# Kernel optimization log

Hardware: AMD Instinct MI355X
Metric: run time of the kernel (lower is better)

## Reference

```python
import jax, jax.numpy as jnp
import numpy as np
from jax import lax

MAX_SIGMA = 20.0
TRUNCATE = 4.0  # scipy.ndimage.gaussian_filter default
R = int(TRUNCATE * MAX_SIGMA + 0.5)  # fixed max radius = 80 -> 161 taps


def setup_inputs() -> dict:
    key = jax.random.key(0)
    k1, k2 = jax.random.split(key)
    x = jax.random.normal(k1, (512, 256, 256), dtype=jnp.float32)
    blur_sigmas = jnp.geomspace(0.5, MAX_SIGMA, 32).astype(jnp.float32)
    fwd_steps = jax.random.randint(k2, (512,), 0, 32)
    return {"x": x, "blur_sigmas": blur_sigmas, "fwd_steps": fwd_steps}


def _per_sample_kernels(sigmas):
    # scipy gaussian_filter: radius_i = int(truncate*sigma + 0.5), kernel
    # phi(o) = exp(-o^2 / (2 sigma^2)) normalized over |o| <= radius_i.
    off = jnp.arange(-R, R + 1, dtype=jnp.float32)          # [2R+1]
    w = jnp.exp(-0.5 * (off[None, :] / sigmas[:, None]) ** 2)  # [B, 2R+1]
    rad = jnp.floor(TRUNCATE * sigmas + 0.5)[:, None]        # per-sample radius
    w = w * (jnp.abs(off)[None, :] <= rad)
    return w / jnp.sum(w, axis=-1, keepdims=True)


def _blur(x, kernels):
    # x: [B, H, W]; kernels: [B, 2R+1]. Separable depthwise conv, batch as
    # channels with feature_group_count=B; symmetric pad == scipy 'reflect'.
    B = x.shape[0]
    dn = ("NCHW", "OIHW", "NCHW")
    xp = jnp.pad(x, ((0, 0), (R, R), (R, R)), mode="symmetric")[None]  # [1,B,H+2R,W+2R]
    kh = kernels[:, None, :, None]  # [B,1,2R+1,1]
    kw = kernels[:, None, None, :]  # [B,1,1,2R+1]
    y = lax.conv_general_dilated(xp, kh, (1, 1), "VALID",
                                 dimension_numbers=dn, feature_group_count=B)
    y = lax.conv_general_dilated(y, kw, (1, 1), "VALID",
                                 dimension_numbers=dn, feature_group_count=B)
    return y[0]  # [B, H, W]


def reference(x, blur_sigmas, fwd_steps):
    sigmas = blur_sigmas[fwd_steps]           # [B] per-sample sigma
    kernels = _per_sample_kernels(sigmas)     # [B, 2R+1]
    return _blur(x, kernels)
```

## Files before the change

### kernel.cpp

```cpp
#include <hip/hip_runtime.h>

#define WDIM  256
#define NSAMP 512
#define NSIG  32
#define NBLK  2048
#define QOFF  16
#define WOFF  65536

typedef float    f32x4 __attribute__((ext_vector_type(4)));
typedef _Float16 f16x4 __attribute__((ext_vector_type(4)));
typedef _Float16 f16x8 __attribute__((ext_vector_type(8)));
typedef __fp16   fp16x2 __attribute__((ext_vector_type(2)));

#define LDS_BARRIER() do {                                         \
    asm volatile("s_waitcnt lgkmcnt(0)" ::: "memory");             \
    __builtin_amdgcn_s_barrier();                                  \
} while (0)

__device__ __forceinline__ int reflect(int q) {
    q = (q < 0) ? (-q - 1) : q;
    return (q >= WDIM) ? (2 * WDIM - 1 - q) : q;
}

__global__ __launch_bounds__(256) void build_all(const float* __restrict__ sigmas,
                                                 const int* __restrict__ steps,
                                                 _Float16* __restrict__ Wg,
                                                 int* __restrict__ q) {
    int t = threadIdx.x;
    if (blockIdx.x < 256) {
        __shared__ float wl[161];
        __shared__ float red;
        int s = blockIdx.x >> 3, og = blockIdx.x & 7;
        float sigma = sigmas[s];
        float radf = floorf(4.0f * sigma + 0.5f);
        if (t < 161) {
            float off = (float)(t - 80);
            float w = 0.0f;
            if (fabsf(off) <= radf) { float z = off / sigma; w = expf(-0.5f * z * z); }
            wl[t] = w;
        }
        __syncthreads();
        if (t < 64) {
            float v = wl[t] + wl[t + 64] + (t < 33 ? wl[t + 128] : 0.0f);
            #pragma unroll
            for (int o = 32; o > 0; o >>= 1) v += __shfl_down(v, o);
            if (t == 0) red = 1.0f / v;
        }
        __syncthreads();
        float rs = red;
        int i = t;
        _Float16* wrow = Wg + ((size_t)s << 16) + (i << 8);
        for (int rq = og * 4; rq < og * 4 + 4; ++rq) {
            f16x8 v;
            #pragma unroll
            for (int j = 0; j < 8; ++j) {
                int r = rq * 8 + j;
                int d1 = r - i, d2 = -r - 1 - i, d3 = 511 - r - i;
                float w = 0.0f;
                if (d1 >= -80 && d1 <= 80) w += wl[d1 + 80];
                if (d2 >= -80)             w += wl[d2 + 80];
                if (d3 <= 80)              w += wl[d3 + 80];
                v[j] = (_Float16)(w * rs);
            }
            *(f16x8*)(wrow + rq * 8) = v;
        }
    } else {
        __shared__ int hist[32];
        __shared__ int base[32];
        if (t < 32) hist[t] = 0;
        __syncthreads();
        int nb2[2], rd2[2], st2[2];
        #pragma unroll
        for (int k = 0; k < 2; ++k) {
            int samp = t + 256 * k;
            int st = steps[samp];
            float sigma = sigmas[st];
            int rad = (int)floorf(4.0f * sigma + 0.5f);
            st2[k] = st; rd2[k] = rad;
            nb2[k] = (2 * rad + 15) >> 3;
            atomicAdd(&hist[nb2[k]], 1);
        }
        __syncthreads();
        if (t == 0) {
            int acc = 0;
            for (int bin = 31; bin >= 0; --bin) { base[bin] = acc; acc += hist[bin]; }
        }
        __syncthreads();
        #pragma unroll
        for (int k = 0; k < 2; ++k) {
            int samp = t + 256 * k;
            int r = atomicAdd(&base[nb2[k]], 1);
            int x = r & 7;
            int p = r >> 3;
            #pragma unroll
            for (int jb = 0; jb < 4; ++jb)
                q[QOFF + (((p << 2) + jb) << 3) + x] =
                    samp | (jb << 9) | (st2[k] << 11) | (rd2[k] << 16);
        }
    }
}

template <bool QUEUED>
__global__ __launch_bounds__(256, 3) void blur_mfma(const float* __restrict__ in,
                                                    float* __restrict__ out,
                                                    const float* __restrict__ sigmas,
                                                    const int* __restrict__ steps,
                                                    const int* __restrict__ q,
                                                    const _Float16* __restrict__ Wg) {
    __shared__ alignas(16) _Float16 XL[256 * 32];
    __shared__ alignas(16) _Float16 WH[64 * 32];
    __shared__ alignas(16) _Float16 YT[64 * 256];

    int b, j0, s, rad;
    if constexpr (QUEUED) {
        int d = q[QOFF + blockIdx.x];
        b   = d & 511;
        j0  = ((d >> 9) & 3) << 6;
        s   = (d >> 11) & 31;
        rad = (d >> 16) & 127;
    } else {
        int bid = blockIdx.x;
        int e = (bid & 7) * (NBLK / 8) + (bid >> 3);
        b = e >> 2; j0 = (e & 3) << 6;
        s = steps[b];
        rad = (int)floorf(4.0f * sigmas[s] + 0.5f);
    }
    const _Float16* Wm = Wg + ((size_t)s << 16);
    const float*    Xb = in + ((size_t)b << 16);

    int tt = threadIdx.x;
    int ln = tt & 63, wv = tt >> 6;
    int lm = ln & 15, lq = ln >> 4;

    int sr = tt >> 3;
    int sc = (tt & 7) * 4;
    int sj = tt >> 2;
    int sw8 = (tt & 3) * 8;

    int kh0 = max(0, j0 - rad) >> 5;
    int kh1 = min(WDIM - 1, j0 + 63 + rad) >> 5;

    f32x4 xs[8];
    f16x8 wst;
    auto ldstage = [&](int kt) {
        const float* xp = Xb + (size_t)sr * WDIM + (kt << 5) + sc;
        #pragma unroll
        for (int k = 0; k < 8; ++k)
            xs[k] = *(const f32x4*)(xp + (size_t)(k * 32) * WDIM);
        wst = *(const f16x8*)(Wm + (size_t)(j0 + sj) * WDIM + (kt << 5) + sw8);
    };
    auto wrstage = [&]() {
        #pragma unroll
        for (int k = 0; k < 8; ++k) {
            int rr = sr + 32 * k;
            union { f16x4 v; fp16x2 h[2]; } u;
            u.h[0] = __builtin_amdgcn_cvt_pkrtz(xs[k][0], xs[k][1]);
            u.h[1] = __builtin_amdgcn_cvt_pkrtz(xs[k][2], xs[k][3]);
            *(f16x4*)&XL[rr * 32 + ((((sc >> 3) ^ (rr & 3)) << 3) + (sc & 7))] = u.v;
        }
        *(f16x8*)&WH[sj * 32 + (((tt & 3) ^ (sj & 3)) << 3)] = wst;
    };

    f32x4 acc[4][4];
    #pragma unroll
    for (int mt = 0; mt < 4; ++mt)
        #pragma unroll
        for (int nt = 0; nt < 4; ++nt) acc[mt][nt] = (f32x4)0.0f;

    ldstage(kh0);
    for (int kt = kh0; kt <= kh1; ++kt) {
        wrstage();
        LDS_BARRIER();
        if (kt < kh1) ldstage(kt + 1);
        f16x8 bf[4];
        #pragma unroll
        for (int nt = 0; nt < 4; ++nt) {
            int j = nt * 16 + lm;
            bf[nt] = *(const f16x8*)&WH[j * 32 + ((lq ^ (j & 3)) << 3)];
        }
        #pragma unroll
        for (int mt = 0; mt < 4; ++mt) {
            int r = wv * 64 + mt * 16 + lm;
            f16x8 af = *(const f16x8*)&XL[r * 32 + ((lq ^ (r & 3)) << 3)];
            #pragma unroll
            for (int nt = 0; nt < 4; ++nt)
                acc[mt][nt] = __builtin_amdgcn_mfma_f32_16x16x32_f16(af, bf[nt], acc[mt][nt], 0, 0, 0);
        }
        LDS_BARRIER();
    }

    #pragma unroll
    for (int mt = 0; mt < 4; ++mt)
        #pragma unroll
        for (int nt = 0; nt < 4; ++nt) {
            int r4 = wv * 64 + mt * 16 + lq * 4;
            int j  = nt * 16 + lm;
            union { f16x4 v; fp16x2 h[2]; } u;
            u.h[0] = __builtin_amdgcn_cvt_pkrtz(acc[mt][nt][0], acc[mt][nt][1]);
            u.h[1] = __builtin_amdgcn_cvt_pkrtz(acc[mt][nt][2], acc[mt][nt][3]);
            *(f16x4*)&YT[j * 256 + ((((r4 >> 3) ^ (j & 7)) << 3) + (r4 & 7))] = u.v;
        }
    LDS_BARRIER();

    f32x4 hac[4][4];
    #pragma unroll
    for (int mt = 0; mt < 4; ++mt)
        #pragma unroll
        for (int nt = 0; nt < 4; ++nt) hac[mt][nt] = (f32x4)0.0f;

    int ka[4], kb[4];
    #pragma unroll
    for (int mt = 0; mt < 4; ++mt) {
        int i0m = wv * 64 + mt * 16;
        ka[mt] = max(0, i0m - rad) >> 5;
        kb[mt] = min(WDIM - 1, i0m + 15 + rad) >> 5;
    }

    for (int kt = ka[0]; kt <= kb[3]; ++kt) {
        f16x8 bf[4];
        #pragma unroll
        for (int nt = 0; nt < 4; ++nt) {
            int j = nt * 16 + lm;
            bf[nt] = *(const f16x8*)&YT[j * 256 + ((((kt << 2) + lq) ^ (j & 7)) << 3)];
        }
        #pragma unroll
        for (int mt = 0; mt < 4; ++mt) {
            if (kt >= ka[mt] && kt <= kb[mt]) {
                f16x8 af = *(const f16x8*)(Wm + (size_t)(wv * 64 + mt * 16 + lm) * WDIM + (kt << 5) + lq * 8);
                #pragma unroll
                for (int nt = 0; nt < 4; ++nt)
                    hac[mt][nt] = __builtin_amdgcn_mfma_f32_16x16x32_f16(af, bf[nt], hac[mt][nt], 0, 0, 0);
            }
        }
    }

    float* ob = out + ((size_t)b << 16);
    #pragma unroll
    for (int mt = 0; mt < 4; ++mt)
        #pragma unroll
        for (int nt = 0; nt < 4; ++nt)
            #pragma unroll
            for (int g = 0; g < 4; ++g)
                ob[(size_t)(wv * 64 + mt * 16 + lq * 4 + g) * WDIM + j0 + nt * 16 + lm] = hac[mt][nt][g];
}

__device__ __forceinline__ int make_weights161(int b, const float* __restrict__ sigmas,
                                               const int* __restrict__ steps,
                                               float* wl, float* red) {
    int t = threadIdx.x;
    float sigma = sigmas[steps[b]];
    float radf = floorf(4.0f * sigma + 0.5f);
    if (t < 192) {
        float w = 0.0f;
        if (t < 161) {
            float off = (float)(t - 80);
            if (fabsf(off) <= radf) { float z = off / sigma; w = expf(-0.5f * z * z); }
        }
        wl[t] = w;
    }
    __syncthreads();
    if (t < 64) {
        float v = wl[t] + wl[t + 64] + wl[t + 128];
        #pragma unroll
        for (int o = 32; o > 0; o >>= 1) v += __shfl_down(v, o);
        if (t == 0) red[0] = 1.0f / v;
    }
    __syncthreads();
    float rs = red[0];
    if (t < 161) wl[t] *= rs;
    __syncthreads();
    return (int)radf;
}

__global__ __launch_bounds__(256) void vblur_nt(const float* __restrict__ in,
                                                float* __restrict__ out,
                                                const float* __restrict__ sigmas,
                                                const int* __restrict__ steps) {
    __shared__ float wl[192];
    __shared__ float red[1];
    int bid = blockIdx.x;
    int b = bid >> 4, i0 = (bid & 15) * 16;
    int rad = make_weights161(b, sigmas, steps, wl, red);
    int j = threadIdx.x;
    const float* inb = in + (size_t)b * WDIM * WDIM;
    float acc[16];
    #pragma unroll
    for (int ii = 0; ii < 16; ++ii) acc[ii] = 0.0f;
    for (int u = -rad; u <= rad; ++u) {
        float w = wl[80 + u];
        #pragma unroll
        for (int ii = 0; ii < 16; ++ii)
            acc[ii] = fmaf(w, inb[reflect(i0 + ii + u) * WDIM + j], acc[ii]);
    }
    #pragma unroll
    for (int ii = 0; ii < 16; ++ii)
        out[((size_t)b * WDIM + (i0 + ii)) * WDIM + j] = acc[ii];
}

__global__ __launch_bounds__(256) void hblur_inplace(float* __restrict__ buf,
                                                     const float* __restrict__ sigmas,
                                                     const int* __restrict__ steps) {
    __shared__ float wl[192];
    __shared__ float red[1];
    __shared__ float rp[WDIM + 160];
    int bid = blockIdx.x;
    int b = bid >> 8, i = bid & 255;
    float* row = buf + ((size_t)b * WDIM + i) * WDIM;
    int t = threadIdx.x;
    for (int s = t; s < WDIM + 160; s += 256) rp[s] = row[reflect(s - 80)];
    int rad = make_weights161(b, sigmas, steps, wl, red);
    float acc = 0.0f;
    for (int u = -rad; u <= rad; ++u) acc = fmaf(wl[80 + u], rp[80 + t + u], acc);
    row[t] = acc;
}

extern "C" void kernel_launch(void* const* d_in, const int* in_sizes, int n_in,
                              void* d_out, int out_size, void* d_ws, size_t ws_size,
                              hipStream_t stream) {
    const float* x     = (const float*)d_in[0];
    const float* sig   = (const float*)d_in[1];
    const int*   steps = (const int*)d_in[2];
    float* out = (float*)d_out;

    const size_t need = (size_t)WOFF + (size_t)NSIG * WDIM * WDIM * 2;
    if (ws_size >= need) {
        int* q = (int*)d_ws;
        _Float16* Wg = (_Float16*)((char*)d_ws + WOFF);
        build_all<<<257, 256, 0, stream>>>(sig, steps, Wg, q);
        blur_mfma<true><<<NBLK, 256, 0, stream>>>(x, out, sig, steps, q, Wg);
    } else {
        vblur_nt<<<NSAMP * 16, 256, 0, stream>>>(x, out, sig, steps);
        hblur_inplace<<<NSAMP * WDIM, 256, 0, stream>>>(out, sig, steps);
    }
}
```

Baseline: 73.62 us.

## Split fused blur into separate horizontal and vertical MFMA kernels via fp16 workspace

The single fused kernel, which kept the horizontal-pass result in LDS and then ran the vertical pass on it, is split into two kernels. The first writes an fp16 intermediate to a global workspace, and the second reads it back to run the vertical pass over its own row tile. Removing the large YT LDS buffer lowers shared-memory use, which allows higher occupancy (launch bounds raised to 4 blocks per CU). In exchange it adds a global round trip of 64 MB (written and read) and a second kernel launch, and it needs a larger workspace; if the workspace is too small, the slow scalar fallback path runs instead.

```diff
diff --git a/kernel.cpp b/kernel.cpp
--- a/kernel.cpp
+++ b/kernel.cpp
@@ -6,6 +6,7 @@
 #define NBLK  2048
 #define QOFF  16
 #define WOFF  65536
+#define TOFF  (WOFF + NSIG * WDIM * WDIM * 2)
 
 typedef float    f32x4 __attribute__((ext_vector_type(4)));
 typedef _Float16 f16x4 __attribute__((ext_vector_type(4)));
@@ -101,23 +102,19 @@
 }
 
 template <bool QUEUED>
-__global__ __launch_bounds__(256, 3) void blur_mfma(const float* __restrict__ in,
-                                                    float* __restrict__ out,
-                                                    const float* __restrict__ sigmas,
-                                                    const int* __restrict__ steps,
-                                                    const int* __restrict__ q,
-                                                    const _Float16* __restrict__ Wg) {
+__global__ __launch_bounds__(256, 4) void blur_h(const float* __restrict__ in,
+                                                 _Float16* __restrict__ tmp,
+                                                 const float* __restrict__ sigmas,
+                                                 const int* __restrict__ steps,
+                                                 const int* __restrict__ q,
+                                                 const _Float16* __restrict__ Wg) {
     __shared__ alignas(16) _Float16 XL[256 * 32];
     __shared__ alignas(16) _Float16 WH[64 * 32];
-    __shared__ alignas(16) _Float16 YT[64 * 256];
 
     int b, j0, s, rad;
     if constexpr (QUEUED) {
         int d = q[QOFF + blockIdx.x];
-        b   = d & 511;
-        j0  = ((d >> 9) & 3) << 6;
-        s   = (d >> 11) & 31;
-        rad = (d >> 16) & 127;
+        b = d & 511; j0 = ((d >> 9) & 3) << 6; s = (d >> 11) & 31; rad = (d >> 16) & 127;
     } else {
         int bid = blockIdx.x;
         int e = (bid & 7) * (NBLK / 8) + (bid >> 3);
@@ -131,7 +128,6 @@
     int tt = threadIdx.x;
     int ln = tt & 63, wv = tt >> 6;
     int lm = ln & 15, lq = ln >> 4;
-
     int sr = tt >> 3;
     int sc = (tt & 7) * 4;
     int sj = tt >> 2;
@@ -189,18 +185,44 @@
         LDS_BARRIER();
     }
 
+    _Float16* tb = tmp + ((size_t)b << 16);
     #pragma unroll
     for (int mt = 0; mt < 4; ++mt)
         #pragma unroll
         for (int nt = 0; nt < 4; ++nt) {
             int r4 = wv * 64 + mt * 16 + lq * 4;
-            int j  = nt * 16 + lm;
+            int j  = j0 + nt * 16 + lm;
             union { f16x4 v; fp16x2 h[2]; } u;
             u.h[0] = __builtin_amdgcn_cvt_pkrtz(acc[mt][nt][0], acc[mt][nt][1]);
             u.h[1] = __builtin_amdgcn_cvt_pkrtz(acc[mt][nt][2], acc[mt][nt][3]);
-            *(f16x4*)&YT[j * 256 + ((((r4 >> 3) ^ (j & 7)) << 3) + (r4 & 7))] = u.v;
-        }
-    LDS_BARRIER();
+            *(f16x4*)&tb[(j << 8) + r4] = u.v;
+        }
+}
+
+template <bool QUEUED>
+__global__ __launch_bounds__(256, 4) void blur_v(const _Float16* __restrict__ tmp,
+                                                 float* __restrict__ out,
+                                                 const float* __restrict__ sigmas,
+                                                 const int* __restrict__ steps,
+                                                 const int* __restrict__ q,
+                                                 const _Float16* __restrict__ Wg) {
+    int b, i0, s, rad;
+    if constexpr (QUEUED) {
+        int d = q[QOFF + blockIdx.x];
+        b = d & 511; i0 = ((d >> 9) & 3) << 6; s = (d >> 11) & 31; rad = (d >> 16) & 127;
+    } else {
+        int bid = blockIdx.x;
+        int e = (bid & 7) * (NBLK / 8) + (bid >> 3);
+        b = e >> 2; i0 = (e & 3) << 6;
+        s = steps[b];
+        rad = (int)floorf(4.0f * sigmas[s] + 0.5f);
+    }
+    const _Float16* Wm = Wg + ((size_t)s << 16);
+    const _Float16* tb = tmp + ((size_t)b << 16);
+
+    int ln = threadIdx.x & 63, wv = threadIdx.x >> 6;
+    int lm = ln & 15, lq = ln >> 4;
+    int jlo = wv * 64;
 
     f32x4 hac[4][4];
     #pragma unroll
@@ -211,22 +233,22 @@
     int ka[4], kb[4];
     #pragma unroll
     for (int mt = 0; mt < 4; ++mt) {
-        int i0m = wv * 64 + mt * 16;
-        ka[mt] = max(0, i0m - rad) >> 5;
-        kb[mt] = min(WDIM - 1, i0m + 15 + rad) >> 5;
+        int im = i0 + mt * 16;
+        ka[mt] = max(0, im - rad) >> 5;
+        kb[mt] = min(WDIM - 1, im + 15 + rad) >> 5;
     }
 
     for (int kt = ka[0]; kt <= kb[3]; ++kt) {
         f16x8 bf[4];
         #pragma unroll
         for (int nt = 0; nt < 4; ++nt) {
-            int j = nt * 16 + lm;
-            bf[nt] = *(const f16x8*)&YT[j * 256 + ((((kt << 2) + lq) ^ (j & 7)) << 3)];
+            int j = jlo + nt * 16 + lm;
+            bf[nt] = *(const f16x8*)&tb[(j << 8) + (kt << 5) + lq * 8];
         }
         #pragma unroll
         for (int mt = 0; mt < 4; ++mt) {
             if (kt >= ka[mt] && kt <= kb[mt]) {
-                f16x8 af = *(const f16x8*)(Wm + (size_t)(wv * 64 + mt * 16 + lm) * WDIM + (kt << 5) + lq * 8);
+                f16x8 af = *(const f16x8*)(Wm + (size_t)(i0 + mt * 16 + lm) * WDIM + (kt << 5) + lq * 8);
                 #pragma unroll
                 for (int nt = 0; nt < 4; ++nt)
                     hac[mt][nt] = __builtin_amdgcn_mfma_f32_16x16x32_f16(af, bf[nt], hac[mt][nt], 0, 0, 0);
@@ -241,7 +263,7 @@
         for (int nt = 0; nt < 4; ++nt)
             #pragma unroll
             for (int g = 0; g < 4; ++g)
-                ob[(size_t)(wv * 64 + mt * 16 + lq * 4 + g) * WDIM + j0 + nt * 16 + lm] = hac[mt][nt][g];
+                ob[(size_t)(i0 + mt * 16 + lq * 4 + g) * WDIM + jlo + nt * 16 + lm] = hac[mt][nt][g];
 }
 
 __device__ __forceinline__ int make_weights161(int b, const float* __restrict__ sigmas,
@@ -322,12 +344,14 @@
     const int*   steps = (const int*)d_in[2];
     float* out = (float*)d_out;
 
-    const size_t need = (size_t)WOFF + (size_t)NSIG * WDIM * WDIM * 2;
+    const size_t need = (size_t)TOFF + (size_t)NSAMP * WDIM * WDIM * 2;
     if (ws_size >= need) {
         int* q = (int*)d_ws;
-        _Float16* Wg = (_Float16*)((char*)d_ws + WOFF);
+        _Float16* Wg  = (_Float16*)((char*)d_ws + WOFF);
+        _Float16* tmp = (_Float16*)((char*)d_ws + TOFF);
         build_all<<<257, 256, 0, stream>>>(sig, steps, Wg, q);
-        blur_mfma<true><<<NBLK, 256, 0, stream>>>(x, out, sig, steps, q, Wg);
+        blur_h<true><<<NBLK, 256, 0, stream>>>(x, tmp, sig, steps, q, Wg);
+        blur_v<true><<<NBLK, 256, 0, stream>>>(tmp, out, sig, steps, q, Wg);
     } else {
         vblur_nt<<<NSAMP * 16, 256, 0, stream>>>(x, out, sig, steps);
         hblur_inplace<<<NSAMP * WDIM, 256, 0, stream>>>(out, sig, steps);
```

Measured after the change: 124.5 us. 1.69x slower.

## Load MFMA operands directly from global memory, dropping LDS staging in first pass

Applied to the files above, without the earlier changes.

The first (vertical-as-GEMM) pass now loads the input rows and the per-sigma weight matrix straight from global memory into MFMA operand registers, instead of staging them through XL/WH shared buffers with double-buffered prefetch and barriers. This removes LDS writes, two barriers per k-tile and 5 KB+ of LDS, which may raise occupancy. In exchange, the software prefetch overlap is lost, each wave issues its own uncoalesced-ish 32-byte row reads, and the weight tile is read redundantly by all four waves, so it leans on the cache.

```diff
diff --git a/kernel.cpp b/kernel.cpp
--- a/kernel.cpp
+++ b/kernel.cpp
@@ -107,17 +107,12 @@
                                                     const int* __restrict__ steps,
                                                     const int* __restrict__ q,
                                                     const _Float16* __restrict__ Wg) {
-    __shared__ alignas(16) _Float16 XL[256 * 32];
-    __shared__ alignas(16) _Float16 WH[64 * 32];
     __shared__ alignas(16) _Float16 YT[64 * 256];
 
     int b, j0, s, rad;
     if constexpr (QUEUED) {
         int d = q[QOFF + blockIdx.x];
-        b   = d & 511;
-        j0  = ((d >> 9) & 3) << 6;
-        s   = (d >> 11) & 31;
-        rad = (d >> 16) & 127;
+        b = d & 511; j0 = ((d >> 9) & 3) << 6; s = (d >> 11) & 31; rad = (d >> 16) & 127;
     } else {
         int bid = blockIdx.x;
         int e = (bid & 7) * (NBLK / 8) + (bid >> 3);
@@ -128,65 +123,41 @@
     const _Float16* Wm = Wg + ((size_t)s << 16);
     const float*    Xb = in + ((size_t)b << 16);
 
-    int tt = threadIdx.x;
-    int ln = tt & 63, wv = tt >> 6;
+    int ln = threadIdx.x & 63, wv = threadIdx.x >> 6;
     int lm = ln & 15, lq = ln >> 4;
 
-    int sr = tt >> 3;
-    int sc = (tt & 7) * 4;
-    int sj = tt >> 2;
-    int sw8 = (tt & 3) * 8;
+    f32x4 acc[4][4];
+    #pragma unroll
+    for (int mt = 0; mt < 4; ++mt)
+        #pragma unroll
+        for (int nt = 0; nt < 4; ++nt) acc[mt][nt] = (f32x4)0.0f;
 
     int kh0 = max(0, j0 - rad) >> 5;
     int kh1 = min(WDIM - 1, j0 + 63 + rad) >> 5;
 
-    f32x4 xs[8];
-    f16x8 wst;
-    auto ldstage = [&](int kt) {
-        const float* xp = Xb + (size_t)sr * WDIM + (kt << 5) + sc;
-        #pragma unroll
-        for (int k = 0; k < 8; ++k)
-            xs[k] = *(const f32x4*)(xp + (size_t)(k * 32) * WDIM);
-        wst = *(const f16x8*)(Wm + (size_t)(j0 + sj) * WDIM + (kt << 5) + sw8);
-    };
-    auto wrstage = [&]() {
-        #pragma unroll
-        for (int k = 0; k < 8; ++k) {
-            int rr = sr + 32 * k;
-            union { f16x4 v; fp16x2 h[2]; } u;
-            u.h[0] = __builtin_amdgcn_cvt_pkrtz(xs[k][0], xs[k][1]);
-            u.h[1] = __builtin_amdgcn_cvt_pkrtz(xs[k][2], xs[k][3]);
-            *(f16x4*)&XL[rr * 32 + ((((sc >> 3) ^ (rr & 3)) << 3) + (sc & 7))] = u.v;
-        }
-        *(f16x8*)&WH[sj * 32 + (((tt & 3) ^ (sj & 3)) << 3)] = wst;
-    };
-
-    f32x4 acc[4][4];
-    #pragma unroll
-    for (int mt = 0; mt < 4; ++mt)
-        #pragma unroll
-        for (int nt = 0; nt < 4; ++nt) acc[mt][nt] = (f32x4)0.0f;
-
-    ldstage(kh0);
     for (int kt = kh0; kt <= kh1; ++kt) {
-        wrstage();
-        LDS_BARRIER();
-        if (kt < kh1) ldstage(kt + 1);
         f16x8 bf[4];
         #pragma unroll
-        for (int nt = 0; nt < 4; ++nt) {
-            int j = nt * 16 + lm;
-            bf[nt] = *(const f16x8*)&WH[j * 32 + ((lq ^ (j & 3)) << 3)];
-        }
+        for (int nt = 0; nt < 4; ++nt)
+            bf[nt] = *(const f16x8*)(Wm + (size_t)(j0 + nt * 16 + lm) * WDIM + (kt << 5) + lq * 8);
+        f32x4 xlo[4], xhi[4];
         #pragma unroll
         for (int mt = 0; mt < 4; ++mt) {
-            int r = wv * 64 + mt * 16 + lm;
-            f16x8 af = *(const f16x8*)&XL[r * 32 + ((lq ^ (r & 3)) << 3)];
+            const float* xp = Xb + (size_t)(wv * 64 + mt * 16 + lm) * WDIM + (kt << 5) + lq * 8;
+            xlo[mt] = *(const f32x4*)xp;
+            xhi[mt] = *(const f32x4*)(xp + 4);
+        }
+        #pragma unroll
+        for (int mt = 0; mt < 4; ++mt) {
+            union { f16x8 v; fp16x2 h[4]; } u;
+            u.h[0] = __builtin_amdgcn_cvt_pkrtz(xlo[mt][0], xlo[mt][1]);
+            u.h[1] = __builtin_amdgcn_cvt_pkrtz(xlo[mt][2], xlo[mt][3]);
+            u.h[2] = __builtin_amdgcn_cvt_pkrtz(xhi[mt][0], xhi[mt][1]);
+            u.h[3] = __builtin_amdgcn_cvt_pkrtz(xhi[mt][2], xhi[mt][3]);
             #pragma unroll
             for (int nt = 0; nt < 4; ++nt)
-                acc[mt][nt] = __builtin_amdgcn_mfma_f32_16x16x32_f16(af, bf[nt], acc[mt][nt], 0, 0, 0);
-        }
-        LDS_BARRIER();
+                acc[mt][nt] = __builtin_amdgcn_mfma_f32_16x16x32_f16(u.v, bf[nt], acc[mt][nt], 0, 0, 0);
+        }
     }
 
     #pragma unroll
```

Result: slower. 90.29 us (+22.6%).
